# Kernel tuning notes

Measured on AMD Instinct MI355X. Metric: run time of the kernel, lower is better.

## Reference

```python
import jax, jax.numpy as jnp
import numpy as np
import math

N = 10000      # num nodes
DEG = 3        # base avg out-degree of random directed graph
D = 128        # d_model
H = 8          # heads
C = D // H     # head dim
L = 2          # num_layers
HOPS = 2       # num_hops


def _build_attn_window(rng):
    # random directed base graph
    E0 = N * DEG
    s0 = rng.integers(0, N, E0).astype(np.int64)
    d0 = rng.integers(0, N, E0).astype(np.int64)
    # to_undirected + coalesce
    s = np.concatenate([s0, d0]); d = np.concatenate([d0, s0])
    key = np.unique(s * N + d)
    s, d = key // N, key % N
    # add self loops (as in _get_attn_window) and coalesce
    loops = np.arange(N, dtype=np.int64)
    key = np.unique(np.concatenate([loops * N + loops, s * N + d]))
    s, d = key // N, key % N
    # base adjacency in CSR-like form grouped by source
    order = np.argsort(s, kind='stable')
    bss, bsd = s[order], d[order]
    outdeg = np.bincount(bss, minlength=N)
    indptr = np.concatenate([[0], np.cumsum(outdeg)])
    # k_hop = A; for _ in range(HOPS-1): k_hop = k_hop @ A   (boolean sparse product)
    cs, cd = s.copy(), d.copy()
    for _ in range(HOPS - 1):
        counts = outdeg[cd]
        total = int(counts.sum())
        new_s = np.repeat(cs, counts)
        starts = np.repeat(indptr[cd], counts)
        offs = np.arange(total, dtype=np.int64) - np.repeat(
            np.concatenate([[0], np.cumsum(counts)])[:-1], counts)
        new_d = bsd[starts + offs]
        key = np.unique(new_s * N + new_d)
        cs, cd = key // N, key % N
    return np.stack([cs, cd]).astype(np.int64)  # [2, E2] (src, dst)


def setup_inputs() -> dict:
    rng = np.random.default_rng(0)
    aw = _build_attn_window(rng)
    key = jax.random.key(0)
    ks = jax.random.split(key, 10)
    sc = 1.0 / math.sqrt(D)
    x = jax.random.normal(ks[0], (N, D), jnp.float32)
    Wq = jax.random.normal(ks[1], (L, D, D), jnp.float32) * sc
    Wk = jax.random.normal(ks[2], (L, D, D), jnp.float32) * sc
    Wv = jax.random.normal(ks[3], (L, D, D), jnp.float32) * sc
    Ws = jax.random.normal(ks[4], (L, D, D), jnp.float32) * sc
    bq = jax.random.normal(ks[5], (L, D), jnp.float32) * 0.01
    bk = jax.random.normal(ks[6], (L, D), jnp.float32) * 0.01
    bv = jax.random.normal(ks[7], (L, D), jnp.float32) * 0.01
    bs = jax.random.normal(ks[8], (L, D), jnp.float32) * 0.01
    return {"x": x, "Wq": Wq, "bq": bq, "Wk": Wk, "bk": bk,
            "Wv": Wv, "bv": bv, "Ws": Ws, "bs": bs,
            "attn_window": jnp.asarray(aw)}


def _segment_softmax(logits, seg):
    # logits: [E, H], seg: [E] destination node ids (every node has a self loop)
    m = jax.ops.segment_max(logits, seg, num_segments=N)
    e = jnp.exp(logits - m[seg])
    z = jax.ops.segment_sum(e, seg, num_segments=N)
    return e / z[seg]


def _transformer_conv(h, wq, bq_, wk, bk_, wv, bv_, ws, bs_, src, dst):
    # PyG TransformerConv (concat=True, root_weight=True, beta=False, eval mode)
    q = (h @ wq + bq_).reshape(N, H, C)
    k = (h @ wk + bk_).reshape(N, H, C)
    v = (h @ wv + bv_).reshape(N, H, C)
    logits = jnp.einsum('ehc,ehc->eh', q[dst], k[src]) * (1.0 / math.sqrt(C))
    alpha = _segment_softmax(logits, dst)                       # [E, H]
    agg = jax.ops.segment_sum(alpha[:, :, None] * v[src], dst,  # [N, H, C]
                              num_segments=N)
    return agg.reshape(N, D) + h @ ws + bs_


def reference(x, Wq, bq, Wk, bk, Wv, bv, Ws, bs, attn_window):
    src, dst = attn_window[0], attn_window[1]
    h = x
    for l in range(L - 1):
        h = jax.nn.relu(h + _transformer_conv(
            h, Wq[l], bq[l], Wk[l], bk[l], Wv[l], bv[l], Ws[l], bs[l], src, dst))
    l = L - 1
    h = h + _transformer_conv(
        h, Wq[l], bq[l], Wk[l], bk[l], Wv[l], bv[l], Ws[l], bs[l], src, dst)
    return h
```

## Files before the change

kernel.cpp:

```cpp
#include <hip/hip_runtime.h>
#include <hip/hip_bf16.h>

typedef __hip_bfloat16 bf16;
typedef __attribute__((ext_vector_type(8))) short bf16x8v;
typedef __attribute__((ext_vector_type(4))) float f32x4v;
typedef __attribute__((ext_vector_type(2))) float f32x2v;

#define N_NODES 10000
#define DMODEL  128
#define NHEADS  8
#define CHEAD   16


#ifndef __has_builtin
#define __has_builtin(x) 0
#endif
#if __has_builtin(__builtin_amdgcn_cvt_pk_f32_fp8) && \
    __has_builtin(__builtin_amdgcn_cvt_pk_fp8_f32)
#define FP8_HW 1
#else
#define FP8_HW 0
#endif

__device__ __forceinline__ float bf2f(unsigned u) {
    union { unsigned i; float f; } c; c.i = u << 16; return c.f;
}
__device__ __forceinline__ unsigned short f2bf_bits(float f) {
    bf16 b = __float2bfloat16(f);
    return *(unsigned short*)&b;
}

__device__ __forceinline__ unsigned char f2fp8(float f) {
#if FP8_HW
    int p = __builtin_amdgcn_cvt_pk_fp8_f32(f, f, 0, false);
    return (unsigned char)(p & 0xff);
#else
    _Float16 hf = (_Float16)f;
    unsigned short u = *reinterpret_cast<unsigned short*>(&hf);
    unsigned s = (u >> 8) & 0x80u;
    unsigned mag = u & 0x7fffu;
    unsigned t = mag + 0x3Fu + ((mag >> 7) & 1u);
    int v = (int)(t >> 7) - 0x40;
    if (v < 0) v = 0;
    if (v > 0x7e) v = 0x7e;
    return (unsigned char)(s | (unsigned)v);
#endif
}
__device__ __forceinline__ void fp8x4_to_f32(unsigned w, float* f) {
#if FP8_HW
    f32x2v lo = __builtin_amdgcn_cvt_pk_f32_fp8((int)w, false);
    f32x2v hi = __builtin_amdgcn_cvt_pk_f32_fp8((int)w, true);
    f[0] = lo[0]; f[1] = lo[1]; f[2] = hi[0]; f[3] = hi[1];
#else
    #pragma unroll
    for (int i = 0; i < 4; ++i) {
        unsigned b = (w >> (8 * i)) & 0xffu;
        unsigned h = ((b & 0x80u) << 8) | (((b & 0x7fu) << 7) + 0x2000u);
        h = (b & 0x7fu) ? h : ((b & 0x80u) << 8);
        unsigned short us = (unsigned short)h;
        _Float16 f16 = *reinterpret_cast<_Float16*>(&us);
        f[i] = (float)f16;
    }
#endif
}

__global__ __launch_bounds__(256) void gemm_qkvs(
    const void* __restrict__ Ain, int a_is_bf16,
    const float* __restrict__ Wq, const float* __restrict__ Wk,
    const float* __restrict__ Wv, const float* __restrict__ Ws,
    const float* __restrict__ bq, const float* __restrict__ bk,
    const float* __restrict__ bv, const float* __restrict__ bs,
    int welem, int belem,
    float* __restrict__ qo, unsigned char* __restrict__ ko,
    bf16* __restrict__ vo, float* __restrict__ hso,
    const int* __restrict__ aw, int E,
    int* __restrict__ rowptr, int* __restrict__ nbr)
{
    __shared__ unsigned short As[64][136];
    __shared__ unsigned short Bs[128][68];
    __shared__ int nz;

    const int tid = threadIdx.x;

    if (E > 0) {
        if (tid == 0) nz = 0;
        __syncthreads();
        int W = 4096;
        if (W > 2 * E) W = 2 * E;
        int any = 0;
        for (int w = 1 + 2 * tid; w < W; w += 2 * (int)blockDim.x)
            any |= aw[w];
        if (any) atomicOr(&nz, 1);
        __syncthreads();
        const int is64 = (nz == 0);

        const int gid = (blockIdx.y * gridDim.x + blockIdx.x) * blockDim.x
                      + tid;
        const int gtot = gridDim.x * gridDim.y * blockDim.x;
        if (gid == 0) rowptr[N_NODES] = E;
        for (int e = gid; e < E; e += gtot) {
            int s  = is64 ? aw[2 * e] : aw[e];
            if (s < 0) s = 0;
            if (s >= N_NODES) s = N_NODES - 1;
            int sp = (e == 0) ? -1 : (is64 ? aw[2 * (e - 1)] : aw[e - 1]);
            for (int r = sp + 1; r <= s; ++r) rowptr[r] = e;
            if (e == E - 1)
                for (int r = s + 1; r < N_NODES; ++r) rowptr[r] = E;
            int d = is64 ? aw[2 * (E + e)] : aw[E + e];
            if (d < 0) d = 0;
            if (d >= N_NODES) d = N_NODES - 1;
            nbr[e] = d;
        }
        __syncthreads();
    }

    const int cb    = blockIdx.x;
    const int row0  = blockIdx.y * 64;
    const int mat   = cb >> 1;
    const float* W    = (mat == 0) ? Wq : (mat == 1) ? Wk
                      : (mat == 2) ? Wv : Ws;
    const float* bias = (mat == 0) ? bq : (mat == 1) ? bk
                      : (mat == 2) ? bv : bs;
    const int colW0 = (cb & 1) * 64;

    if (a_is_bf16) {
        const unsigned short* A = (const unsigned short*)Ain;
        #pragma unroll
        for (int i = 0; i < 4; ++i) {
            int idx = tid + i * 256;
            int row = idx >> 4, k8 = idx & 15;
            int grow = row0 + row;
            uint4 u = make_uint4(0u, 0u, 0u, 0u);
            if (grow < N_NODES)
                u = *(const uint4*)&A[grow * DMODEL + k8 * 8];
            *(uint4*)&As[row][k8 * 8] = u;
        }
    } else {
        const float* A = (const float*)Ain;
        #pragma unroll
        for (int i = 0; i < 8; ++i) {
            int idx = tid + i * 256;
            int row = idx >> 5, k4 = idx & 31;
            int grow = row0 + row;
            float4 av = make_float4(0.f, 0.f, 0.f, 0.f);
            if (grow < N_NODES)
                av = *(const float4*)&A[grow * DMODEL + k4 * 4];
            ushort4 p;
            p.x = f2bf_bits(av.x); p.y = f2bf_bits(av.y);
            p.z = f2bf_bits(av.z); p.w = f2bf_bits(av.w);
            *(ushort4*)&As[row][k4 * 4] = p;
        }
    }
    #pragma unroll
    for (int i = 0; i < 8; ++i) {
        int idx = tid + i * 256;
        int kk = idx >> 4, n4 = idx & 15;
        float4 wv = *(const float4*)&W[welem + kk * DMODEL + colW0 + n4 * 4];
        ushort4 p;
        p.x = f2bf_bits(wv.x); p.y = f2bf_bits(wv.y);
        p.z = f2bf_bits(wv.z); p.w = f2bf_bits(wv.w);
        *(ushort4*)&Bs[kk][n4 * 4] = p;
    }
    __syncthreads();

    const int wave = tid >> 6, lane = tid & 63;
    const int ln = lane & 15, quad = lane >> 4;
    const int ncol = wave * 16 + ln;

    f32x4v acc[4];
    #pragma unroll
    for (int mt = 0; mt < 4; ++mt) acc[mt] = (f32x4v){0.f, 0.f, 0.f, 0.f};

    #pragma unroll
    for (int ks = 0; ks < 4; ++ks) {
        const int kb = ks * 32 + quad * 8;
        bf16x8v bfv;
        #pragma unroll
        for (int j = 0; j < 8; ++j) bfv[j] = (short)Bs[kb + j][ncol];
        #pragma unroll
        for (int mt = 0; mt < 4; ++mt) {
            bf16x8v afv = *(const bf16x8v*)&As[mt * 16 + ln][kb];
            acc[mt] = __builtin_amdgcn_mfma_f32_16x16x32_bf16(
                afv, bfv, acc[mt], 0, 0, 0);
        }
    }

    const float bcol = bias[belem + colW0 + ncol];
    #pragma unroll
    for (int mt = 0; mt < 4; ++mt) {
        #pragma unroll
        for (int r = 0; r < 4; ++r) {
            int row = row0 + mt * 16 + quad * 4 + r;
            if (row >= N_NODES) continue;
            float val = acc[mt][r] + bcol;
            int elo = row * DMODEL + colW0 + ncol;
            if (mat == 0)      qo[elo] = val;
            else if (mat == 3) hso[elo] = val;
            else if (mat == 1) ko[elo] = f2fp8(val);
            else               vo[elo] = __float2bfloat16(val);
        }
    }
}

__global__ __launch_bounds__(128) void attn_fused(
    const float* __restrict__ q, const unsigned char* __restrict__ k,
    const bf16* __restrict__ v, const float* __restrict__ hs,
    const float* __restrict__ hin_f,
    const unsigned short* __restrict__ hin_b,
    const int* __restrict__ rowptr, const int* __restrict__ nbr,
    float* __restrict__ out, unsigned short* __restrict__ outb,
    int relu_flag)
{
    __shared__ float lacc[2][64][2];
    __shared__ float lz[2][64];

    const int wv = threadIdx.x >> 6;
    const int l = threadIdx.x & 63;
    const int h = l & 7, slot = l >> 3;
    const int hc = l >> 3;

    const int d = blockIdx.x;

    float qf[16];
    const float* qp = q + d * DMODEL + h * CHEAD;
    #pragma unroll
    for (int i = 0; i < 4; ++i) {
        float4 t4 = *(const float4*)(qp + i * 4);
        qf[i * 4 + 0] = t4.x; qf[i * 4 + 1] = t4.y;
        qf[i * 4 + 2] = t4.z; qf[i * 4 + 3] = t4.w;
    }

    const int e0 = rowptr[d], e1 = rowptr[d + 1];
    float zacc = 0.f;
    float2 acc = make_float2(0.f, 0.f);

    const int start = e0 + wv * 8;
    int eg = start + slot;
    bool pad_cur = !(eg < e1);
    int s_cur = pad_cur ? d : nbr[eg];
    uint4 kc = *(const uint4*)(k + s_cur * DMODEL + h * CHEAD);

    for (int base = start; base < e1; base += 16) {
        int en = base + 16 + slot;
        bool pad_nxt = !(en < e1);
        int s_nxt = pad_nxt ? d : nbr[en];
        uint4 kn = *(const uint4*)(k + s_nxt * DMODEL + h * CHEAD);

        int se[8];
        #pragma unroll
        for (int e = 0; e < 8; ++e) se[e] = __shfl(s_cur, e * 8);
        unsigned uv[8];
        #pragma unroll
        for (int e = 0; e < 8; ++e)
            uv[e] = *(const unsigned*)(v + se[e] * DMODEL + 2 * l);

        const unsigned* kw = (const unsigned*)&kc;
        float dot = 0.f;
        #pragma unroll
        for (int w = 0; w < 4; ++w) {
            float kf[4];
            fp8x4_to_f32(kw[w], kf);
            dot += qf[w * 4 + 0] * kf[0];
            dot += qf[w * 4 + 1] * kf[1];
            dot += qf[w * 4 + 2] * kf[2];
            dot += qf[w * 4 + 3] * kf[3];
        }
        float p = pad_cur ? -3.0e38f : fminf(dot * 0.25f, 60.f);
        float pe = __expf(p);
        zacc += pe;

        float pee[8];
        #pragma unroll
        for (int e = 0; e < 8; ++e) pee[e] = __shfl(pe, e * 8 + hc);
        #pragma unroll
        for (int e = 0; e < 8; ++e) {
            acc.x += pee[e] * bf2f(uv[e] & 0xffffu);
            acc.y += pee[e] * bf2f(uv[e] >> 16);
        }

        kc = kn; s_cur = s_nxt; pad_cur = pad_nxt;
    }

    lacc[wv][l][0] = acc.x; lacc[wv][l][1] = acc.y; lz[wv][l] = zacc;
    __syncthreads();
    const int ow = wv ^ 1;
    acc.x += lacc[ow][l][0];
    acc.y += lacc[ow][l][1];
    zacc  += lz[ow][l];

    float z = zacc;
    z += __shfl_xor(z, 8);
    z += __shfl_xor(z, 16);
    z += __shfl_xor(z, 32);
    float zh = __shfl(z, hc);
    float inv = (zh > 0.f) ? (1.f / zh) : 0.f;

    const bool do_f32 = (out  != 0) && (wv == 0);
    const bool do_bf  = (outb != 0) && (wv == 1);
    if (do_f32 || do_bf) {
        int idx = d * DMODEL + 2 * l;
        float2 hsv = *(const float2*)(hs + idx);
        float2 hiv;
        if (hin_f) {
            hiv = *(const float2*)(hin_f + idx);
        } else {
            unsigned u = *(const unsigned*)(hin_b + idx);
            hiv.x = bf2f(u & 0xffffu);
            hiv.y = bf2f(u >> 16);
        }
        float2 o;
        o.x = acc.x * inv + hsv.x + hiv.x;
        o.y = acc.y * inv + hsv.y + hiv.y;
        if (relu_flag) { o.x = fmaxf(o.x, 0.f); o.y = fmaxf(o.y, 0.f); }
        if (do_f32) *(float2*)(out + idx) = o;
        if (do_bf) {
            unsigned pk = f2bf_bits(o.x) | ((unsigned)f2bf_bits(o.y) << 16);
            *(unsigned*)&outb[idx] = pk;
        }
    }
}

extern "C" void kernel_launch(void* const* d_in, const int* in_sizes, int n_in,
                              void* d_out, int out_size, void* d_ws, size_t ws_size,
                              hipStream_t stream) {
    const float* x  = (const float*)d_in[0];
    const float* Wq = (const float*)d_in[1];
    const float* bq = (const float*)d_in[2];
    const float* Wk = (const float*)d_in[3];
    const float* bk = (const float*)d_in[4];
    const float* Wv = (const float*)d_in[5];
    const float* bv = (const float*)d_in[6];
    const float* Ws = (const float*)d_in[7];
    const float* bs = (const float*)d_in[8];
    const int*   aw = (const int*)d_in[9];
    const int E = in_sizes[9] / 2;

    char* ws = (char*)d_ws;
    size_t off = 0;
    float* qb = (float*)(ws + off);  off += (size_t)N_NODES * DMODEL * 4;
    unsigned char* kb = (unsigned char*)(ws + off);
    off += (size_t)N_NODES * DMODEL;
    off = (off + 255) & ~(size_t)255;
    bf16*  vb = (bf16*)(ws + off);   off += (size_t)N_NODES * DMODEL * 2;
    float* hsb = (float*)(ws + off); off += (size_t)N_NODES * DMODEL * 4;
    unsigned short* h1b = (unsigned short*)(ws + off);
    off += (size_t)N_NODES * DMODEL * 2;
    int* rowptr = (int*)(ws + off);  off += ((size_t)N_NODES + 2) * 4;
    int* nbr    = (int*)(ws + off);  off += (size_t)E * 4;

    dim3 ggrid(8, (N_NODES + 63) / 64);

    gemm_qkvs<<<ggrid, 256, 0, stream>>>(x, 0, Wq, Wk, Wv, Ws,
                                         bq, bk, bv, bs, 0, 0,
                                         qb, kb, vb, hsb, aw, E, rowptr, nbr);
    attn_fused<<<N_NODES, 128, 0, stream>>>(qb, kb, vb, hsb, x,
                                            (const unsigned short*)0,
                                            rowptr, nbr,
                                            (float*)0, h1b, 1);
    gemm_qkvs<<<ggrid, 256, 0, stream>>>(h1b, 1, Wq, Wk, Wv, Ws,
                                         bq, bk, bv, bs,
                                         DMODEL * DMODEL, DMODEL,
                                         qb, kb, vb, hsb, aw, 0, rowptr, nbr);
    attn_fused<<<N_NODES, 128, 0, stream>>>(qb, kb, vb, hsb,
                                            (const float*)0, h1b,
                                            rowptr, nbr,
                                            (float*)d_out,
                                            (unsigned short*)0, 0);
}
```

Measured before the change: 154.6 us.

## Have each lane own one edge-head and accumulate full V head slice

```diff
diff --git a/kernel.cpp b/kernel.cpp
--- a/kernel.cpp
+++ b/kernel.cpp
@@ -211,13 +211,12 @@
     float* __restrict__ out, unsigned short* __restrict__ outb,
     int relu_flag)
 {
-    __shared__ float lacc[2][64][2];
-    __shared__ float lz[2][64];
+    __shared__ float part[16][132];
+    __shared__ float lzw[2][8];
 
     const int wv = threadIdx.x >> 6;
     const int l = threadIdx.x & 63;
     const int h = l & 7, slot = l >> 3;
-    const int hc = l >> 3;
 
     const int d = blockIdx.x;
 
@@ -232,68 +231,78 @@
 
     const int e0 = rowptr[d], e1 = rowptr[d + 1];
     float zacc = 0.f;
-    float2 acc = make_float2(0.f, 0.f);
+    float acc[16];
+    #pragma unroll
+    for (int j = 0; j < 16; ++j) acc[j] = 0.f;
 
     const int start = e0 + wv * 8;
-    int eg = start + slot;
-    bool pad_cur = !(eg < e1);
-    int s_cur = pad_cur ? d : nbr[eg];
-    uint4 kc = *(const uint4*)(k + s_cur * DMODEL + h * CHEAD);
-
-    for (int base = start; base < e1; base += 16) {
-        int en = base + 16 + slot;
-        bool pad_nxt = !(en < e1);
-        int s_nxt = pad_nxt ? d : nbr[en];
-        uint4 kn = *(const uint4*)(k + s_nxt * DMODEL + h * CHEAD);
-
-        int se[8];
-        #pragma unroll
-        for (int e = 0; e < 8; ++e) se[e] = __shfl(s_cur, e * 8);
-        unsigned uv[8];
-        #pragma unroll
-        for (int e = 0; e < 8; ++e)
-            uv[e] = *(const unsigned*)(v + se[e] * DMODEL + 2 * l);
-
-        const unsigned* kw = (const unsigned*)&kc;
-        float dot = 0.f;
-        #pragma unroll
-        for (int w = 0; w < 4; ++w) {
-            float kf[4];
-            fp8x4_to_f32(kw[w], kf);
-            dot += qf[w * 4 + 0] * kf[0];
-            dot += qf[w * 4 + 1] * kf[1];
-            dot += qf[w * 4 + 2] * kf[2];
-            dot += qf[w * 4 + 3] * kf[3];
-        }
-        float p = pad_cur ? -3.0e38f : fminf(dot * 0.25f, 60.f);
-        float pe = __expf(p);
-        zacc += pe;
-
-        float pee[8];
-        #pragma unroll
-        for (int e = 0; e < 8; ++e) pee[e] = __shfl(pe, e * 8 + hc);
-        #pragma unroll
-        for (int e = 0; e < 8; ++e) {
-            acc.x += pee[e] * bf2f(uv[e] & 0xffffu);
-            acc.y += pee[e] * bf2f(uv[e] >> 16);
-        }
-
-        kc = kn; s_cur = s_nxt; pad_cur = pad_nxt;
-    }
-
-    lacc[wv][l][0] = acc.x; lacc[wv][l][1] = acc.y; lz[wv][l] = zacc;
-    __syncthreads();
-    const int ow = wv ^ 1;
-    acc.x += lacc[ow][l][0];
-    acc.y += lacc[ow][l][1];
-    zacc  += lz[ow][l];
+    {
+        int eg = start + slot;
+        bool pad_cur = !(eg < e1);
+        int s_cur = pad_cur ? d : nbr[eg];
+        uint4 kc = *(const uint4*)(k + s_cur * DMODEL + h * CHEAD);
+        const uint4* vp = (const uint4*)(v + s_cur * DMODEL + h * CHEAD);
+        uint4 vc0 = vp[0], vc1 = vp[1];
+
+        for (int base = start; base < e1; base += 16) {
+            int en = base + 16 + slot;
+            bool pad_nxt = !(en < e1);
+            int s_nxt = pad_nxt ? d : nbr[en];
+            uint4 kn = *(const uint4*)(k + s_nxt * DMODEL + h * CHEAD);
+            const uint4* vpn = (const uint4*)(v + s_nxt * DMODEL + h * CHEAD);
+            uint4 vn0 = vpn[0], vn1 = vpn[1];
+
+            const unsigned* kw = (const unsigned*)&kc;
+            float dot = 0.f;
+            #pragma unroll
+            for (int w = 0; w < 4; ++w) {
+                float kf[4];
+                fp8x4_to_f32(kw[w], kf);
+                dot += qf[w * 4 + 0] * kf[0];
+                dot += qf[w * 4 + 1] * kf[1];
+                dot += qf[w * 4 + 2] * kf[2];
+                dot += qf[w * 4 + 3] * kf[3];
+            }
+            float p = pad_cur ? -3.0e38f : fminf(dot * 0.25f, 60.f);
+            float pe = __expf(p);
+            zacc += pe;
+
+            const unsigned* vw0 = (const unsigned*)&vc0;
+            const unsigned* vw1 = (const unsigned*)&vc1;
+            #pragma unroll
+            for (int w = 0; w < 4; ++w) {
+                acc[2 * w + 0] += pe * bf2f(vw0[w] & 0xffffu);
+                acc[2 * w + 1] += pe * bf2f(vw0[w] >> 16);
+                acc[8 + 2 * w + 0] += pe * bf2f(vw1[w] & 0xffffu);
+                acc[8 + 2 * w + 1] += pe * bf2f(vw1[w] >> 16);
+            }
+
+            kc = kn; vc0 = vn0; vc1 = vn1; pad_cur = pad_nxt;
+        }
+    }
 
     float z = zacc;
     z += __shfl_xor(z, 8);
     z += __shfl_xor(z, 16);
     z += __shfl_xor(z, 32);
-    float zh = __shfl(z, hc);
-    float inv = (zh > 0.f) ? (1.f / zh) : 0.f;
+    if (l < 8) lzw[wv][l] = z;
+
+    const int p = wv * 8 + slot;
+    #pragma unroll
+    for (int i = 0; i < 4; ++i)
+        *(float4*)&part[p][h * CHEAD + i * 4] =
+            make_float4(acc[i * 4 + 0], acc[i * 4 + 1],
+                        acc[i * 4 + 2], acc[i * 4 + 3]);
+    __syncthreads();
+
+    float ax = 0.f, ay = 0.f;
+    #pragma unroll
+    for (int i = 0; i < 16; ++i) {
+        float2 t = *(const float2*)&part[i][2 * l];
+        ax += t.x; ay += t.y;
+    }
+    float zt = lzw[0][l >> 3] + lzw[1][l >> 3];
+    float inv = (zt > 0.f) ? (1.f / zt) : 0.f;
 
     const bool do_f32 = (out  != 0) && (wv == 0);
     const bool do_bf  = (outb != 0) && (wv == 1);
@@ -309,8 +318,8 @@
             hiv.y = bf2f(u >> 16);
         }
         float2 o;
-        o.x = acc.x * inv + hsv.x + hiv.x;
-        o.y = acc.y * inv + hsv.y + hiv.y;
+        o.x = ax * inv + hsv.x + hiv.x;
+        o.y = ay * inv + hsv.y + hiv.y;
         if (relu_flag) { o.x = fmaxf(o.x, 0.f); o.y = fmaxf(o.y, 0.f); }
         if (do_f32) *(float2*)(out + idx) = o;
         if (do_bf) {
```

Result: faster. 148.9 us, median of 2 (-3.7%).
